# Optimization experiments

Measured on AMD Instinct MI355X. Metric: run time of the kernel, lower is better.

## Reference

```python
import jax, jax.numpy as jnp
import numpy as np

EPS = 1e-8  # torch F.cosine_similarity eps


def _wn(v, g):
    # torch weight_norm: w = g * v / ||v|| (norm per output channel, over input dim)
    return g[:, None] * v / jnp.linalg.norm(v, axis=1, keepdims=True)


def setup_inputs() -> dict:
    key = jax.random.key(0)
    ks = jax.random.split(key, 8)
    N, C, L = 4, 512, 4096     # batch, input channels, flattened spatial/time
    D, K = 256, 8192           # code channels, num codes
    x = jax.random.normal(ks[0], (N, C, L), jnp.float32)
    in_v = jax.random.normal(ks[1], (D, C), jnp.float32) / np.sqrt(C).astype(np.float32)
    in_g = jnp.linalg.norm(in_v, axis=1)            # weight_norm init: g = ||v||
    in_b = (jax.random.uniform(ks[2], (D,), jnp.float32) - 0.5) / np.sqrt(C).astype(np.float32)
    out_v = jax.random.normal(ks[3], (C, D), jnp.float32) / np.sqrt(D).astype(np.float32)
    out_g = jnp.linalg.norm(out_v, axis=1)
    out_b = (jax.random.uniform(ks[4], (C,), jnp.float32) - 0.5) / np.sqrt(D).astype(np.float32)
    codebook = jax.random.normal(ks[5], (K, D), jnp.float32)
    return {"x": x, "in_v": in_v, "in_g": in_g, "in_b": in_b,
            "out_v": out_v, "out_g": out_g, "out_b": out_b, "codebook": codebook}


def reference(x, in_v, in_g, in_b, out_v, out_g, out_b, codebook):
    # input 1x1 conv (pointwise linear over channels)
    W_in = _wn(in_v, in_g)                                   # (D, C)
    z_e = jnp.einsum('ncl,dc->ndl', x, W_in) + in_b[None, :, None]  # (N, D, L)

    # cosine-similarity codebook search
    ze_t = z_e.transpose(0, 2, 1)                            # (N, L, D)
    ze_n = ze_t / jnp.maximum(jnp.linalg.norm(ze_t, axis=-1, keepdims=True), EPS)
    cb_n = codebook / jnp.maximum(jnp.linalg.norm(codebook, axis=-1, keepdims=True), EPS)
    sim = jnp.einsum('nld,kd->nlk', ze_n, cb_n)              # (N, L, K) large intermediate
    code_index = jnp.argmax(sim, axis=-1)                    # (N, L) int
    z_q = codebook[code_index].transpose(0, 2, 1)            # (N, D, L)

    # per-sample VQ losses
    cb_loss = jnp.mean((z_q - jax.lax.stop_gradient(z_e)) ** 2, axis=(1, 2))
    cm_loss = jnp.mean((z_e - jax.lax.stop_gradient(z_q)) ** 2, axis=(1, 2))

    # straight-through estimator (training mode); numerically equal to z_q
    z_q_st = jax.lax.stop_gradient(z_q) + (z_e - jax.lax.stop_gradient(z_e))

    # output 1x1 conv
    W_out = _wn(out_v, out_g)                                # (C, D)
    y = jnp.einsum('ndl,cd->ncl', z_q_st, W_out) + out_b[None, :, None]  # (N, C, L)
    return y, code_index, cb_loss, cm_loss
```

## Files before the change

### kernel.cpp

```cpp
#include <hip/hip_runtime.h>
#include <math.h>

#define N_ 4
#define C_ 512
#define L_ 4096
#define D_ 256
#define K_ 8192
#define NL_ 16384

#define OUT_IDX_OFF (N_*C_*L_)
#define OUT_CB_OFF  (OUT_IDX_OFF + NL_)

#define WS_ZT   0
#define WS_P    (WS_ZT + (size_t)NL_*D_)
#define WS_Z2   (WS_P + (size_t)K_*C_)
#define WS_CB2  (WS_Z2 + (size_t)NL_*D_)
#define WS_PART (WS_CB2 + (size_t)K_*D_)
#define WS_WIN  (WS_PART + (size_t)NL_*64*4)
#define WS_WOUT (WS_WIN + (size_t)D_*C_)
#define WS_INVN (WS_WOUT + (size_t)C_*D_)
#define WS_IDX  (WS_INVN + (size_t)K_)
#define WS_LOSS (WS_IDX + (size_t)NL_)

typedef __bf16 bf16x8 __attribute__((ext_vector_type(8)));
typedef float  f32x4  __attribute__((ext_vector_type(4)));
typedef unsigned int u32;

__device__ __forceinline__ unsigned short f2bf(float f) {
    u32 u = __float_as_uint(f);
    u32 r = (u + 0x7fffu + ((u >> 16) & 1u)) >> 16;
    return (unsigned short)r;
}
__device__ __forceinline__ float bf2f(unsigned short h) {
    return __uint_as_float(((u32)h) << 16);
}

__device__ __forceinline__ float waveReduceSum64(float s) {
    #pragma unroll
    for (int off = 32; off; off >>= 1) s += __shfl_xor(s, off, 64);
    return s;
}

__device__ __forceinline__ bool pref(float av, int ai, float bv, int bi) {
    return (av > bv) || (av == bv && ai < bi);
}
__device__ __forceinline__ void push2(float& v1, int& i1, float& v2, int& i2,
                                      float wv, int wi) {
    if (pref(wv, wi, v1, i1)) { v2 = v1; i2 = i1; v1 = wv; i1 = wi; }
    else if (pref(wv, wi, v2, i2)) { v2 = wv; i2 = wi; }
}

__device__ __forceinline__ void gload_lds16(const void* g, void* l) {
    __builtin_amdgcn_global_load_lds(
        (const __attribute__((address_space(1))) void*)g,
        (__attribute__((address_space(3))) void*)l,
        16, 0, 0);
}

__global__ __launch_bounds__(64) void prep_kernel(
    const float* __restrict__ in_v, const float* __restrict__ in_g,
    const float* __restrict__ out_v, const float* __restrict__ out_g,
    float* __restrict__ Win, float* __restrict__ Wout,
    float* __restrict__ lossacc)
{
    const int b = blockIdx.x;
    const int t = threadIdx.x;
    if (b == 0 && t < N_) lossacc[t] = 0.0f;
    if (b < D_) {
        const float* v = in_v + (size_t)b * C_;
        float4 a0 = *(const float4*)(v + t * 4);
        float4 a1 = *(const float4*)(v + 256 + t * 4);
        float s = a0.x*a0.x + a0.y*a0.y + a0.z*a0.z + a0.w*a0.w
                + a1.x*a1.x + a1.y*a1.y + a1.z*a1.z + a1.w*a1.w;
        s = waveReduceSum64(s);
        float scale = in_g[b] / sqrtf(s);
        float* w = Win + (size_t)b * C_;
        float4 o0, o1;
        o0.x=a0.x*scale; o0.y=a0.y*scale; o0.z=a0.z*scale; o0.w=a0.w*scale;
        o1.x=a1.x*scale; o1.y=a1.y*scale; o1.z=a1.z*scale; o1.w=a1.w*scale;
        *(float4*)(w + t*4) = o0;
        *(float4*)(w + 256 + t*4) = o1;
    } else {
        const int r = b - D_;
        const float* v = out_v + (size_t)r * D_;
        float4 a0 = *(const float4*)(v + t * 4);
        float s = a0.x*a0.x + a0.y*a0.y + a0.z*a0.z + a0.w*a0.w;
        s = waveReduceSum64(s);
        float scale = out_g[r] / sqrtf(s);
        float4 o0;
        o0.x=a0.x*scale; o0.y=a0.y*scale; o0.z=a0.z*scale; o0.w=a0.w*scale;
        *(float4*)(Wout + (size_t)r * D_ + t*4) = o0;
    }
}

__global__ __launch_bounds__(64) void cb2_kernel(
    const float* __restrict__ cb, float* __restrict__ invn)
{
    const int k = blockIdx.x;
    const int t = threadIdx.x;
    float4 v = *(const float4*)(cb + (size_t)k * D_ + t * 4);
    float s = v.x*v.x + v.y*v.y + v.z*v.z + v.w*v.w;
    s = waveReduceSum64(s);
    if (t == 0) invn[k] = 1.0f / fmaxf(sqrtf(s), 1e-8f);
}

__global__ __launch_bounds__(256) void cb2f_kernel(
    const float* __restrict__ cb, const float* __restrict__ invn,
    unsigned short* __restrict__ CB2F)
{
    const int c16 = blockIdx.x;
    const int t = threadIdx.x;
    const int kc = t >> 4, nl = t & 15;
    const int code = c16 * 16 + nl;
    const float inv = invn[code];
    const float* src = cb + (size_t)code * D_ + (kc & 7) * 32;
    unsigned short* dst = CB2F + ((size_t)(c16 * 16 + kc) * 64) * 8;
    #pragma unroll
    for (int lh = 0; lh < 4; ++lh) {
        float4 x0 = *(const float4*)(src + lh * 8);
        float4 x1 = *(const float4*)(src + lh * 8 + 4);
        float f[8] = {x0.x, x0.y, x0.z, x0.w, x1.x, x1.y, x1.z, x1.w};
        unsigned short o[8];
        #pragma unroll
        for (int j = 0; j < 8; ++j) {
            float v = f[j] * inv;
            unsigned short h = f2bf(v);
            o[j] = (kc < 8) ? h : f2bf(v - bf2f(h));
        }
        unsigned short* dp = dst + (lh * 16 + nl) * 8;
        *(ushort4*)&dp[0] = make_ushort4(o[0], o[1], o[2], o[3]);
        *(ushort4*)&dp[4] = make_ushort4(o[4], o[5], o[6], o[7]);
    }
}

__global__ __launch_bounds__(256) void ze_kernel(
    const float* __restrict__ x, const float* __restrict__ Win,
    const float* __restrict__ inb, float* __restrict__ Zt,
    unsigned short* __restrict__ Z2)
{
    __shared__ float Al[2][16][64];
    __shared__ float Bl[2][16][68];
    const int tid = threadIdx.x;
    const int ty = tid >> 4, tx = tid & 15;
    const int l0 = blockIdx.x * 64;
    const int d0 = blockIdx.y * 64;
    const int n  = blockIdx.z;
    const float* xn = x + (size_t)n * C_ * L_;

    const int ac = tid >> 4, alq = tid & 15;
    const int bd = tid >> 2, bq  = tid & 3;

    float acc[4][4];
    #pragma unroll
    for (int i = 0; i < 4; ++i)
        #pragma unroll
        for (int j = 0; j < 4; ++j) acc[i][j] = 0.0f;

    auto stage = [&](int cc, int buf) {
        float4 av = *(const float4*)(xn + (size_t)(cc*16 + ac) * L_ + l0 + alq*4);
        *(float4*)&Al[buf][ac][alq*4] = av;
        float4 bv = *(const float4*)(Win + (size_t)(d0 + bd) * C_ + cc*16 + bq*4);
        Bl[buf][bq*4+0][bd] = bv.x; Bl[buf][bq*4+1][bd] = bv.y;
        Bl[buf][bq*4+2][bd] = bv.z; Bl[buf][bq*4+3][bd] = bv.w;
    };

    stage(0, 0);
    for (int cc = 0; cc < 32; ++cc) {
        __syncthreads();
        if (cc + 1 < 32) stage(cc + 1, (cc + 1) & 1);
        const int buf = cc & 1;
        #pragma unroll
        for (int k = 0; k < 16; ++k) {
            float4 a = *(const float4*)&Al[buf][k][ty*4];
            float4 b = *(const float4*)&Bl[buf][k][tx*4];
            acc[0][0]=fmaf(a.x,b.x,acc[0][0]); acc[0][1]=fmaf(a.x,b.y,acc[0][1]);
            acc[0][2]=fmaf(a.x,b.z,acc[0][2]); acc[0][3]=fmaf(a.x,b.w,acc[0][3]);
            acc[1][0]=fmaf(a.y,b.x,acc[1][0]); acc[1][1]=fmaf(a.y,b.y,acc[1][1]);
            acc[1][2]=fmaf(a.y,b.z,acc[1][2]); acc[1][3]=fmaf(a.y,b.w,acc[1][3]);
            acc[2][0]=fmaf(a.z,b.x,acc[2][0]); acc[2][1]=fmaf(a.z,b.y,acc[2][1]);
            acc[2][2]=fmaf(a.z,b.z,acc[2][2]); acc[2][3]=fmaf(a.z,b.w,acc[2][3]);
            acc[3][0]=fmaf(a.w,b.x,acc[3][0]); acc[3][1]=fmaf(a.w,b.y,acc[3][1]);
            acc[3][2]=fmaf(a.w,b.z,acc[3][2]); acc[3][3]=fmaf(a.w,b.w,acc[3][3]);
        }
    }
    float4 bias = *(const float4*)(inb + d0 + tx*4);
    #pragma unroll
    for (int i = 0; i < 4; ++i) {
        float4 o;
        o.x = acc[i][0] + bias.x; o.y = acc[i][1] + bias.y;
        o.z = acc[i][2] + bias.z; o.w = acc[i][3] + bias.w;
        const size_t row = (size_t)(n*L_ + l0 + ty*4 + i);
        *(float4*)&Zt[row * D_ + d0 + tx*4] = o;
        ushort4 h, lo;
        h.x = f2bf(o.x); h.y = f2bf(o.y); h.z = f2bf(o.z); h.w = f2bf(o.w);
        lo.x = f2bf(o.x - bf2f(h.x)); lo.y = f2bf(o.y - bf2f(h.y));
        lo.z = f2bf(o.z - bf2f(h.z)); lo.w = f2bf(o.w - bf2f(h.w));
        *(ushort4*)&Z2[row * 512 + d0 + tx*4]       = h;
        *(ushort4*)&Z2[row * 512 + 256 + d0 + tx*4] = lo;
    }
}

__global__ __launch_bounds__(256) void pmat_kernel(
    const float* __restrict__ cb, const float* __restrict__ Wout,
    float* __restrict__ P)
{
    __shared__ float Al[2][16][68];
    __shared__ float Bl[2][16][68];
    const int tid = threadIdx.x;
    const int ty = tid >> 4, tx = tid & 15;
    const int k0 = blockIdx.x * 64;
    const int c0 = blockIdx.y * 64;
    const int ar = tid >> 2, aq = tid & 3;

    float acc[4][4];
    #pragma unroll
    for (int i = 0; i < 4; ++i)
        #pragma unroll
        for (int j = 0; j < 4; ++j) acc[i][j] = 0.0f;

    auto stage = [&](int dc, int buf) {
        float4 av = *(const float4*)(cb + (size_t)(k0 + ar) * D_ + dc*16 + aq*4);
        Al[buf][aq*4+0][ar] = av.x; Al[buf][aq*4+1][ar] = av.y;
        Al[buf][aq*4+2][ar] = av.z; Al[buf][aq*4+3][ar] = av.w;
        float4 bv = *(const float4*)(Wout + (size_t)(c0 + ar) * D_ + dc*16 + aq*4);
        Bl[buf][aq*4+0][ar] = bv.x; Bl[buf][aq*4+1][ar] = bv.y;
        Bl[buf][aq*4+2][ar] = bv.z; Bl[buf][aq*4+3][ar] = bv.w;
    };

    stage(0, 0);
    for (int dc = 0; dc < 16; ++dc) {
        __syncthreads();
        if (dc + 1 < 16) stage(dc + 1, (dc + 1) & 1);
        const int buf = dc & 1;
        #pragma unroll
        for (int k = 0; k < 16; ++k) {
            float4 a = *(const float4*)&Al[buf][k][ty*4];
            float4 b = *(const float4*)&Bl[buf][k][tx*4];
            acc[0][0]=fmaf(a.x,b.x,acc[0][0]); acc[0][1]=fmaf(a.x,b.y,acc[0][1]);
            acc[0][2]=fmaf(a.x,b.z,acc[0][2]); acc[0][3]=fmaf(a.x,b.w,acc[0][3]);
            acc[1][0]=fmaf(a.y,b.x,acc[1][0]); acc[1][1]=fmaf(a.y,b.y,acc[1][1]);
            acc[1][2]=fmaf(a.y,b.z,acc[1][2]); acc[1][3]=fmaf(a.y,b.w,acc[1][3]);
            acc[2][0]=fmaf(a.z,b.x,acc[2][0]); acc[2][1]=fmaf(a.z,b.y,acc[2][1]);
            acc[2][2]=fmaf(a.z,b.z,acc[2][2]); acc[2][3]=fmaf(a.z,b.w,acc[2][3]);
            acc[3][0]=fmaf(a.w,b.x,acc[3][0]); acc[3][1]=fmaf(a.w,b.y,acc[3][1]);
            acc[3][2]=fmaf(a.w,b.z,acc[3][2]); acc[3][3]=fmaf(a.w,b.w,acc[3][3]);
        }
    }
    #pragma unroll
    for (int i = 0; i < 4; ++i) {
        float4 o;
        o.x = acc[i][0]; o.y = acc[i][1]; o.z = acc[i][2]; o.w = acc[i][3];
        *(float4*)&P[(size_t)(k0 + ty*4 + i) * C_ + c0 + tx*4] = o;
    }
}

__global__ __launch_bounds__(256, 2) void sim_kernel(
    const unsigned short* __restrict__ Z2, const unsigned short* __restrict__ CB2F,
    float* __restrict__ Part)
{
    __shared__ char lds[4][16384];
    const int tid = threadIdx.x;
    const int w = tid >> 6, l = tid & 63;
    const int bid = blockIdx.x;
    const int ks = bid & 3;
    const int mtile = bid >> 2;
    const int m0 = mtile * 64 + w * 16;
    const int n0 = ks * 2048;
    const char* Bchunk = (const char*)CB2F + (size_t)(n0 >> 4) * 16384;

    const char* Abase = (const char*)Z2 + (size_t)(m0 + (l & 15)) * 1024
                        + ((l >> 4) * 16);
    bf16x8 af[16];
    #pragma unroll
    for (int f = 0; f < 8; ++f) {
        af[f]     = *(const volatile bf16x8*)(Abase + f * 64);
        af[f + 8] = *(const volatile bf16x8*)(Abase + 512 + f * 64);
    }
    asm volatile("s_waitcnt vmcnt(0)" ::: "memory");

    float bv1[4], bv2[4]; int bi1[4], bi2[4];
    #pragma unroll
    for (int t = 0; t < 4; ++t) {
        bv1[t] = -3.0e38f; bv2[t] = -3.0e38f;
        bi1[t] = 0x7FFFFFFF; bi2[t] = 0x7FFFFFFF;
    }

    auto stage = [&](int ch) {
        const char* s = Bchunk + (size_t)ch * 16384 + (size_t)w * 4096
                        + (size_t)l * 16;
        char* d = &lds[ch & 3][w * 4096];
        gload_lds16(s,        d);
        gload_lds16(s + 1024, d + 1024);
        gload_lds16(s + 2048, d + 2048);
        gload_lds16(s + 3072, d + 3072);
    };

    stage(0); stage(1); stage(2);

    for (int c = 0; c < 128; ++c) {
        if (c <= 125)      { asm volatile("s_waitcnt vmcnt(8)" ::: "memory"); }
        else if (c == 126) { asm volatile("s_waitcnt vmcnt(4)" ::: "memory"); }
        else               { asm volatile("s_waitcnt vmcnt(0)" ::: "memory"); }
        __builtin_amdgcn_s_barrier();
        __builtin_amdgcn_sched_barrier(0);
        if (c + 3 < 128) stage(c + 3);

        const char* p = &lds[c & 3][l * 16];
        bf16x8 bg[16];
        #pragma unroll
        for (int f = 0; f < 16; ++f)
            bg[f] = *(const bf16x8*)(p + (size_t)f * 1024);

        f32x4 a0 = {0.f,0.f,0.f,0.f}, a1 = a0, a2 = a0, a3 = a0;
        #pragma unroll
        for (int f = 0; f < 8; f += 2) {
            a0 = __builtin_amdgcn_mfma_f32_16x16x32_bf16(af[f],   bg[f],   a0, 0,0,0);
            a1 = __builtin_amdgcn_mfma_f32_16x16x32_bf16(af[f+1], bg[f+1], a1, 0,0,0);
            a2 = __builtin_amdgcn_mfma_f32_16x16x32_bf16(af[f+8], bg[f],   a2, 0,0,0);
            a3 = __builtin_amdgcn_mfma_f32_16x16x32_bf16(af[f+9], bg[f+1], a3, 0,0,0);
            a0 = __builtin_amdgcn_mfma_f32_16x16x32_bf16(af[f],   bg[f+8], a0, 0,0,0);
            a1 = __builtin_amdgcn_mfma_f32_16x16x32_bf16(af[f+1], bg[f+9], a1, 0,0,0);
        }
        f32x4 s01 = a0 + a1, s23 = a2 + a3;
        f32x4 s = s01 + s23;

        const int colbase = n0 + c * 16 + (l & 15);
        #pragma unroll
        for (int t = 0; t < 4; ++t)
            push2(bv1[t], bi1[t], bv2[t], bi2[t], s[t], colbase);
    }

    #pragma unroll
    for (int t = 0; t < 4; ++t) {
        float v1 = bv1[t], v2 = bv2[t];
        int   i1 = bi1[t], i2 = bi2[t];
        #pragma unroll
        for (int mask = 1; mask < 16; mask <<= 1) {
            float ov1 = __shfl_xor(v1, mask, 64);
            int   oi1 = __shfl_xor(i1, mask, 64);
            float ov2 = __shfl_xor(v2, mask, 64);
            int   oi2 = __shfl_xor(i2, mask, 64);
            push2(v1, i1, v2, i2, ov1, oi1);
            push2(v1, i1, v2, i2, ov2, oi2);
        }
        if ((l & 15) == 0) {
            const int row = m0 + (l >> 4) * 4 + t;
            float4 o;
            o.x = v1; o.y = __int_as_float(i1);
            o.z = v2; o.w = __int_as_float(i2);
            *(float4*)&Part[((size_t)row * 4 + ks) * 4] = o;
        }
    }
}

__global__ __launch_bounds__(256) void argmax_kernel(
    const float* __restrict__ Part, const float* __restrict__ Zt,
    const float* __restrict__ cb, const float* __restrict__ invn,
    int* __restrict__ idxout, float* __restrict__ fidxout)
{
    const int w = threadIdx.x >> 6, l = threadIdx.x & 63;
    const int row = blockIdx.x * 4 + w;
    float v1 = -3.0e38f, v2 = -3.0e38f;
    int   i1 = 0x7FFFFFFF, i2 = 0x7FFFFFFF;
    if (l < 4) {
        float4 p = *(const float4*)&Part[((size_t)row * 4 + l) * 4];
        v1 = p.x; i1 = __float_as_int(p.y);
        v2 = p.z; i2 = __float_as_int(p.w);
    }
    #pragma unroll
    for (int mask = 1; mask < 4; mask <<= 1) {
        float ov1 = __shfl_xor(v1, mask, 64);
        int   oi1 = __shfl_xor(i1, mask, 64);
        float ov2 = __shfl_xor(v2, mask, 64);
        int   oi2 = __shfl_xor(i2, mask, 64);
        push2(v1, i1, v2, i2, ov1, oi1);
        push2(v1, i1, v2, i2, ov2, oi2);
    }
    v1 = __shfl(v1, 0, 64); i1 = __shfl(i1, 0, 64);
    v2 = __shfl(v2, 0, 64); i2 = __shfl(i2, 0, 64);
    const float* z  = Zt + (size_t)row * D_;
    float4 zv = *(const float4*)(z + l*4);
    float4 a  = *(const float4*)(cb + (size_t)i1 * D_ + l*4);
    float4 b  = *(const float4*)(cb + (size_t)i2 * D_ + l*4);
    float s1 = zv.x*a.x + zv.y*a.y + zv.z*a.z + zv.w*a.w;
    float s2 = zv.x*b.x + zv.y*b.y + zv.z*b.z + zv.w*b.w;
    s1 = waveReduceSum64(s1);
    s2 = waveReduceSum64(s2);
    float e1 = s1 * invn[i1];
    float e2 = s2 * invn[i2];
    int win = (e2 > e1 || (e2 == e1 && i2 < i1)) ? i2 : i1;
    if (l == 0) { idxout[row] = win; fidxout[row] = (float)win; }
}

__global__ __launch_bounds__(256) void loss_kernel(
    const float* __restrict__ Zt, const float* __restrict__ cb,
    const int* __restrict__ idx, float* __restrict__ lossacc)
{
    __shared__ float red[4];
    const int tid = threadIdx.x;
    const int r = blockIdx.x * 64 + (tid >> 2);
    const int q = tid & 3;
    const int n = r >> 12;
    const int code = idx[r];
    const float* zp = Zt + (size_t)r * D_ + q * 64;
    const float* cp = cb + (size_t)code * D_ + q * 64;
    float s = 0.0f;
    #pragma unroll
    for (int it = 0; it < 16; ++it) {
        float4 a = *(const float4*)(zp + it*4);
        float4 c = *(const float4*)(cp + it*4);
        float dx = c.x - a.x, dy = c.y - a.y, dz = c.z - a.z, dw = c.w - a.w;
        s += dx*dx + dy*dy + dz*dz + dw*dw;
    }
    s = waveReduceSum64(s);
    if ((tid & 63) == 0) red[tid >> 6] = s;
    __syncthreads();
    if (tid == 0) atomicAdd(&lossacc[n], red[0] + red[1] + red[2] + red[3]);
}

__global__ __launch_bounds__(256) void y_kernel(
    const float* __restrict__ P, const int* __restrict__ idx,
    const float* __restrict__ outb, float* __restrict__ y)
{
    __shared__ float bias[128];
    const int t = threadIdx.x;
    const int c0 = blockIdx.y * 128;
    const int n = blockIdx.z;
    const int l = blockIdx.x * 256 + t;
    if (t < 128) bias[t] = outb[c0 + t];
    __syncthreads();
    const int code = idx[n * L_ + l];
    const float* prow = P + (size_t)code * C_ + c0;
    float* yb = y + ((size_t)n * C_ + c0) * L_ + l;
    #pragma unroll 4
    for (int c = 0; c < 128; ++c) {
        yb[(size_t)c * L_] = prow[c] + bias[c];
    }
}

__global__ __launch_bounds__(64) void fin_kernel(
    const float* __restrict__ lossacc, float* __restrict__ out)
{
    const int t = threadIdx.x;
    if (t < 8) out[t] = lossacc[t & 3] * (1.0f / (float)(D_ * L_));
}

extern "C" void kernel_launch(void* const* d_in, const int* in_sizes, int n_in,
                              void* d_out, int out_size, void* d_ws, size_t ws_size,
                              hipStream_t stream) {
    (void)in_sizes; (void)n_in; (void)out_size; (void)ws_size;
    const float* x     = (const float*)d_in[0];
    const float* in_v  = (const float*)d_in[1];
    const float* in_g  = (const float*)d_in[2];
    const float* in_b  = (const float*)d_in[3];
    const float* out_v = (const float*)d_in[4];
    const float* out_g = (const float*)d_in[5];
    const float* out_b = (const float*)d_in[6];
    const float* cb    = (const float*)d_in[7];
    float* out = (float*)d_out;
    float* ws  = (float*)d_ws;

    float*          Zt     = ws + WS_ZT;
    float*          P      = ws + WS_P;
    unsigned short* Z2     = (unsigned short*)(ws + WS_Z2);
    unsigned short* CB2F   = (unsigned short*)(ws + WS_CB2);
    float*          Part   = ws + WS_PART;
    float*          Win    = ws + WS_WIN;
    float*          Wout   = ws + WS_WOUT;
    float*          invn   = ws + WS_INVN;
    int*            idx    = (int*)(ws + WS_IDX);
    float*          lossac = ws + WS_LOSS;

    prep_kernel<<<dim3(D_ + C_), 64, 0, stream>>>(in_v, in_g, out_v, out_g,
                                                  Win, Wout, lossac);
    cb2_kernel<<<dim3(K_), 64, 0, stream>>>(cb, invn);
    cb2f_kernel<<<dim3(512), 256, 0, stream>>>(cb, invn, CB2F);
    ze_kernel<<<dim3(64, 4, 4), 256, 0, stream>>>(x, Win, in_b, Zt, Z2);
    pmat_kernel<<<dim3(128, 8), 256, 0, stream>>>(cb, Wout, P);
    sim_kernel<<<dim3(1024), 256, 0, stream>>>(Z2, CB2F, Part);
    argmax_kernel<<<dim3(4096), 256, 0, stream>>>(Part, Zt, cb, invn,
                                                  idx, out + OUT_IDX_OFF);
    loss_kernel<<<dim3(256), 256, 0, stream>>>(Zt, cb, idx, lossac);
    y_kernel<<<dim3(16, 4, 4), 256, 0, stream>>>(P, idx, out_b, out);
    fin_kernel<<<dim3(1), 64, 0, stream>>>(lossac, out + OUT_CB_OFF);
}
```

Before: 755.5 us.

## Switch sim kernel to double-buffered LDS with higher occupancy

The codebook similarity kernel drops its 4-deep asynchronous LDS prefetch ring, which used manual vmcnt waits, and uses a 2-buffer ping-pong with __syncthreads instead. This halves LDS per block and raises the launch-bounds occupancy target from 2 to 4 blocks per CU. The B fragments are now read from LDS inside the MFMA loop rather than preloaded into 16 registers, which cuts register pressure so the higher occupancy can fit. The trade is a shallower prefetch and a full block barrier every chunk, with more resident waves expected to hide the latency instead.

Result: faster. 621.8 us (-17.7%).

```diff
diff --git a/kernel.cpp b/kernel.cpp
--- a/kernel.cpp
+++ b/kernel.cpp
@@ -254,11 +254,11 @@
     }
 }
 
-__global__ __launch_bounds__(256, 2) void sim_kernel(
+__global__ __launch_bounds__(256, 4) void sim_kernel(
     const unsigned short* __restrict__ Z2, const unsigned short* __restrict__ CB2F,
     float* __restrict__ Part)
 {
-    __shared__ char lds[4][16384];
+    __shared__ char lds[2][16384];
     const int tid = threadIdx.x;
     const int w = tid >> 6, l = tid & 63;
     const int bid = blockIdx.x;
@@ -276,7 +276,6 @@
         af[f]     = *(const volatile bf16x8*)(Abase + f * 64);
         af[f + 8] = *(const volatile bf16x8*)(Abase + 512 + f * 64);
     }
-    asm volatile("s_waitcnt vmcnt(0)" ::: "memory");
 
     float bv1[4], bv2[4]; int bi1[4], bi2[4];
     #pragma unroll
@@ -285,41 +284,37 @@
         bi1[t] = 0x7FFFFFFF; bi2[t] = 0x7FFFFFFF;
     }
 
-    auto stage = [&](int ch) {
+    auto stage = [&](int ch, int buf) {
         const char* s = Bchunk + (size_t)ch * 16384 + (size_t)w * 4096
                         + (size_t)l * 16;
-        char* d = &lds[ch & 3][w * 4096];
+        char* d = &lds[buf][w * 4096];
         gload_lds16(s,        d);
         gload_lds16(s + 1024, d + 1024);
         gload_lds16(s + 2048, d + 2048);
         gload_lds16(s + 3072, d + 3072);
     };
 
-    stage(0); stage(1); stage(2);
+    stage(0, 0);
+    __syncthreads();
 
     for (int c = 0; c < 128; ++c) {
-        if (c <= 125)      { asm volatile("s_waitcnt vmcnt(8)" ::: "memory"); }
-        else if (c == 126) { asm volatile("s_waitcnt vmcnt(4)" ::: "memory"); }
-        else               { asm volatile("s_waitcnt vmcnt(0)" ::: "memory"); }
-        __builtin_amdgcn_s_barrier();
-        __builtin_amdgcn_sched_barrier(0);
-        if (c + 3 < 128) stage(c + 3);
-
-        const char* p = &lds[c & 3][l * 16];
-        bf16x8 bg[16];
-        #pragma unroll
-        for (int f = 0; f < 16; ++f)
-            bg[f] = *(const bf16x8*)(p + (size_t)f * 1024);
-
+        const int buf = c & 1;
+        if (c + 1 < 128) stage(c + 1, buf ^ 1);
+
+        const char* p = &lds[buf][l * 16];
         f32x4 a0 = {0.f,0.f,0.f,0.f}, a1 = a0, a2 = a0, a3 = a0;
         #pragma unroll
         for (int f = 0; f < 8; f += 2) {
-            a0 = __builtin_amdgcn_mfma_f32_16x16x32_bf16(af[f],   bg[f],   a0, 0,0,0);
-            a1 = __builtin_amdgcn_mfma_f32_16x16x32_bf16(af[f+1], bg[f+1], a1, 0,0,0);
-            a2 = __builtin_amdgcn_mfma_f32_16x16x32_bf16(af[f+8], bg[f],   a2, 0,0,0);
-            a3 = __builtin_amdgcn_mfma_f32_16x16x32_bf16(af[f+9], bg[f+1], a3, 0,0,0);
-            a0 = __builtin_amdgcn_mfma_f32_16x16x32_bf16(af[f],   bg[f+8], a0, 0,0,0);
-            a1 = __builtin_amdgcn_mfma_f32_16x16x32_bf16(af[f+1], bg[f+9], a1, 0,0,0);
+            bf16x8 bh0 = *(const bf16x8*)(p + (size_t)f * 1024);
+            bf16x8 bl0 = *(const bf16x8*)(p + (size_t)(f + 8) * 1024);
+            a0 = __builtin_amdgcn_mfma_f32_16x16x32_bf16(af[f],   bh0, a0, 0,0,0);
+            a1 = __builtin_amdgcn_mfma_f32_16x16x32_bf16(af[f+8], bh0, a1, 0,0,0);
+            a2 = __builtin_amdgcn_mfma_f32_16x16x32_bf16(af[f],   bl0, a2, 0,0,0);
+            bf16x8 bh1 = *(const bf16x8*)(p + (size_t)(f + 1) * 1024);
+            bf16x8 bl1 = *(const bf16x8*)(p + (size_t)(f + 9) * 1024);
+            a3 = __builtin_amdgcn_mfma_f32_16x16x32_bf16(af[f+1], bh1, a3, 0,0,0);
+            a0 = __builtin_amdgcn_mfma_f32_16x16x32_bf16(af[f+9], bh1, a0, 0,0,0);
+            a1 = __builtin_amdgcn_mfma_f32_16x16x32_bf16(af[f+1], bl1, a1, 0,0,0);
         }
         f32x4 s01 = a0 + a1, s23 = a2 + a3;
         f32x4 s = s01 + s23;
@@ -328,6 +323,8 @@
         #pragma unroll
         for (int t = 0; t < 4; ++t)
             push2(bv1[t], bi1[t], bv2[t], bi2[t], s[t], colbase);
+
+        __syncthreads();
     }
 
     #pragma unroll
```
